# Optimization experiments

Hardware: AMD Instinct MI355X
Metric: run time of the kernel (lower is better)

## Reference

```python
import jax, jax.numpy as jnp
import numpy as np
from jax import lax

S = 16  # encoder stride (patchify-conv stand-in for the CNN backbone, stride-16 feature grid)


def _conv(x, w, b, stride, padding):
    y = lax.conv_general_dilated(x, w, (stride, stride), padding,
                                 dimension_numbers=('NCHW', 'OIHW', 'NCHW'))
    return y + b[None, :, None, None]


def _l2norm(x, eps=1e-12):  # F.normalize(p=2, dim=1)
    n = jnp.sqrt(jnp.sum(x * x, axis=1, keepdims=True))
    return x / jnp.maximum(n, eps)


def _encode(frame, ew, eb, kw, kb, vw, vb, mask=None):
    feat = jax.nn.relu(_conv(frame, ew, eb, S, 'VALID'))  # [B,512,h,w]
    key = _conv(feat, kw, kb, 1, 'SAME')                  # [B,64,h,w]
    val = _conv(feat, vw, vb, 1, 'SAME')                  # [B,ed,h,w]
    if mask is not None:
        m = mask[:, None, ::S, ::S]  # torch F.interpolate 'nearest' with exact integer factor
        key = key * m
        val = val * m
    return _l2norm(key), val, feat


def _forward(query_frame, prev_frame, prev_mask, first_frame, first_mask,
             enc_q_w, enc_q_b, enc_m_w, enc_m_b,
             key_w, key_b, val_w, val_b,
             dec1_w, dec1_b, dec2_w, dec2_b, cls_w, cls_b):
    # memory bank reset + push(first), push(prev)
    k1, v1, _ = _encode(first_frame, enc_m_w, enc_m_b, key_w, key_b, val_w, val_b, first_mask)
    kp, vp, _ = _encode(prev_frame, enc_m_w, enc_m_b, key_w, key_b, val_w, val_b, prev_mask)
    qk, qv, _ = _encode(query_frame, enc_q_w, enc_q_b, key_w, key_b, val_w, val_b)
    B, Ck, h, w = qk.shape
    ed = qv.shape[1]
    mem_key = jnp.concatenate([k1.reshape(B, Ck, -1), kp.reshape(B, Ck, -1)], axis=2)  # [B,64,M]
    mem_val = jnp.concatenate([v1.reshape(B, ed, -1), vp.reshape(B, ed, -1)], axis=2)  # [B,ed,M]
    q_key = qk.reshape(B, Ck, -1)                                                      # [B,64,Q]
    # STM memory read: affinity -> softmax -> weighted sum over memory pixels
    affinity = jnp.einsum('bcq,bcm->bqm', q_key, mem_key) / jnp.sqrt(jnp.float32(Ck))
    affinity = jax.nn.softmax(affinity, axis=-1)
    mem_read = jnp.einsum('bqm,bcm->bcq', affinity, mem_val).reshape(B, ed, h, w)
    fused = jnp.concatenate([qv, mem_read], axis=1)  # [B,2*ed,h,w] (aspp=False)
    d = jax.nn.relu(_conv(fused, dec1_w, dec1_b, 1, 'SAME'))
    dec_feat = jax.nn.relu(_conv(d, dec2_w, dec2_b, 1, 'SAME'))
    logits = _conv(dec_feat, cls_w, cls_b, 1, 'SAME')
    H, W = query_frame.shape[-2], query_frame.shape[-1]
    logits_full = jax.image.resize(logits, (B, logits.shape[1], H, W), method='bilinear')  # align_corners=False
    rep_feat = _l2norm(dec_feat)
    return rep_feat, logits_full


def setup_inputs():
    key = jax.random.key(0)
    ks = jax.random.split(key, 16)
    B, H, W = 8, 512, 512
    Ce, Ck, ed = 512, 64, 256
    g = lambda i, sh, s: jax.random.normal(ks[i], sh, dtype=jnp.float32) * s
    return {
        'query_frame': g(0, (B, 3, H, W), 1.0),
        'prev_frame': g(1, (B, 3, H, W), 1.0),
        'prev_mask': jnp.round(jax.random.uniform(ks[2], (B, H, W), dtype=jnp.float32)),
        'first_frame': g(3, (B, 3, H, W), 1.0),
        'first_mask': jnp.round(jax.random.uniform(ks[4], (B, H, W), dtype=jnp.float32)),
        'enc_q_w': g(5, (Ce, 3, S, S), 0.02), 'enc_q_b': jnp.zeros((Ce,), jnp.float32),
        'enc_m_w': g(6, (Ce, 3, S, S), 0.02), 'enc_m_b': jnp.zeros((Ce,), jnp.float32),
        'key_w': g(7, (Ck, Ce, 1, 1), 0.05), 'key_b': jnp.zeros((Ck,), jnp.float32),
        'val_w': g(8, (ed, Ce, 1, 1), 0.05), 'val_b': jnp.zeros((ed,), jnp.float32),
        'dec1_w': g(9, (ed, 2 * ed, 3, 3), 0.02), 'dec1_b': jnp.zeros((ed,), jnp.float32),
        'dec2_w': g(10, (ed, ed, 3, 3), 0.02), 'dec2_b': jnp.zeros((ed,), jnp.float32),
        'cls_w': g(11, (2, ed, 1, 1), 0.05), 'cls_b': jnp.zeros((2,), jnp.float32),
    }


def reference(query_frame, prev_frame, prev_mask, first_frame, first_mask,
              enc_q_w, enc_q_b, enc_m_w, enc_m_b,
              key_w, key_b, val_w, val_b,
              dec1_w, dec1_b, dec2_w, dec2_b, cls_w, cls_b):
    return _forward(query_frame, prev_frame, prev_mask, first_frame, first_mask,
                    enc_q_w, enc_q_b, enc_m_w, enc_m_b,
                    key_w, key_b, val_w, val_b,
                    dec1_w, dec1_b, dec2_w, dec2_b, cls_w, cls_b)
```

## Files before the change

kernel.cpp:

```cpp
#include <hip/hip_runtime.h>
#include <hip/hip_bf16.h>
#include <cstdint>

#define DEV __device__ __forceinline__
typedef __attribute__((ext_vector_type(8))) short short8;
typedef __attribute__((ext_vector_type(4))) float f32x4;
typedef unsigned short u16;

DEV float b2f(u16 u) { union { unsigned int i; float f; } x; x.i = (unsigned)u << 16; return x.f; }
DEV u16 f2b(float f) { __hip_bfloat16 h = __float2bfloat16(f); return *(u16*)&h; }
DEV float rdin(const void* p, size_t i, int isbf) {
  return isbf ? __bfloat162float(((const __hip_bfloat16*)p)[i]) : ((const float*)p)[i];
}
DEV void wrout(void* p, size_t i, float v, int isbf) {
  if (isbf) ((__hip_bfloat16*)p)[i] = __float2bfloat16(v);
  else      ((float*)p)[i] = v;
}
DEV short8 ld8(const void* p, size_t idx, int isbf) {
  if (isbf) return *(const short8*)((const u16*)p + idx);
  const float* f = (const float*)p + idx;
  float4 x = *(const float4*)f, y = *(const float4*)(f + 4);
  short8 r;
  r[0] = f2b(x.x); r[1] = f2b(x.y); r[2] = f2b(x.z); r[3] = f2b(x.w);
  r[4] = f2b(y.x); r[5] = f2b(y.y); r[6] = f2b(y.z); r[7] = f2b(y.w);
  return r;
}

__global__ __launch_bounds__(256) void detect_k(const u16* w, int* flag) {
  __shared__ int cnt[256];
  int tid = threadIdx.x, c = 0;
  for (int i = tid; i < 4096; i += 256) {
    u16 v = w[i];
    int e = (v >> 7) & 0xFF;
    if (v == 0 || (e >= 0x60 && e <= 0x9F)) c++;
  }
  cnt[tid] = c;
  __syncthreads();
  for (int s = 128; s > 0; s >>= 1) { if (tid < s) cnt[tid] += cnt[tid + s]; __syncthreads(); }
  if (tid == 0) *flag = (cnt[0] > 3600) ? 1 : 0;
}

__global__ __launch_bounds__(256) void patchify_k(const void* F0, const void* F1,
                                                  u16* dst, const int* dflag) {
  int isbf = *dflag;
  int bid = blockIdx.x;
  int z = bid >> 8, rem = bid & 255, b = rem >> 5, y = rem & 31;
  const void* F = z ? F1 : F0;
  int x = threadIdx.x & 31, pj = threadIdx.x >> 5;
  u16* drow = dst + (size_t)(z * 8192 + b * 1024 + y * 32 + x) * 768;
#pragma unroll
  for (int i = 0; i < 6; i++) {
    int pair = i * 8 + pj;
    int c = pair >> 4, ky = pair & 15;
    size_t src = ((size_t)((b * 3 + c) * 512 + y * 16 + ky)) * 512 + x * 16;
    short8 v0 = ld8(F, src, isbf);
    short8 v1 = ld8(F, src + 8, isbf);
    u16* dp = drow + c * 256 + ky * 16;
    *(short8*)dp = v0;
    *(short8*)(dp + 8) = v1;
  }
}

__global__ __launch_bounds__(256) void wconv_k(const void* wm, const void* wq,
                                               u16* dst, const int* dflag) {
  int isbf = *dflag;
  size_t e0 = ((size_t)blockIdx.x * 256 + threadIdx.x) * 8;
  const void* src = e0 < 393216 ? wm : wq;
  size_t off = e0 < 393216 ? e0 : e0 - 393216;
  *(short8*)&dst[e0] = ld8(src, off, isbf);
}

struct PA {
  const void* W0; const void* W1; size_t bs; int K; int rowsplit; int zsel; int ws16; int rowmax1;
  DEV short8 l8(int row, int k, int b, int zz, int isbf) const {
    const void* W = W0; int r = row;
    if (zsel && zz == 2) W = W1;
    else if (rowsplit && row >= rowsplit) { W = W1; r = row - rowsplit; if (r > rowmax1) r = rowmax1; }
    return ld8(W, (size_t)b * bs + (size_t)r * K + k, ws16 ? 1 : isbf);
  }
};
struct PBws {
  const u16* X; int rs; size_t zs;
  DEV short8 l8(int t, int k, int zz, int) const {
    return *(const short8*)(X + (size_t)zz * zs + (size_t)t * rs + k);
  }
};
struct PBc3 {
  const u16* X; int C; int shift;
  DEV short8 l8(int t, int k, int, int) const {
    int tap = k >> shift, c0 = k & (C - 1);
    int dy = tap / 3, dx = tap - dy * 3;
    int pos = t & 1023, y = pos >> 5, x = pos & 31;
    int iy = y + dy - 1, ix = x + dx - 1;
    if ((unsigned)iy >= 32u || (unsigned)ix >= 32u) { short8 z = {0,0,0,0,0,0,0,0}; return z; }
    return *(const short8*)(X + (size_t)(((t >> 10) * 1024) + iy * 32 + ix) * C + c0);
  }
};

struct Epi {
  int mode;
  u16 *o16, *o16b, *o16c;
  size_t zs; int ts, moff, mmax;
  const void *bias, *bias2; int bzsel;
  const void *maskA, *maskB;
  const float* rscale;
  float scale; int relu, doexp;
  DEV void store1(int m, int t, int z, float v, int isbf) const {
    if (m >= mmax) return;
    int b = t >> 10, pos = t & 1023;
    if (m < 256) {
      v += rdin(bias, m, isbf);
      if (z < 2) {
        const void* mk = z ? maskB : maskA;
        v *= rdin(mk, ((size_t)(b * 512 + (pos >> 5) * 16) << 9) + (pos & 31) * 16, isbf);
        o16[((size_t)(b * 256 + m)) * 2048 + (size_t)z * 1024 + pos] = f2b(v);
      } else {
        o16b[(size_t)t * 512 + m] = f2b(v);
      }
    } else {
      v += rdin(bias2, m - 256, isbf);
      o16c[((size_t)z * 8192 + t) * 64 + (m - 256)] = f2b(v);
    }
  }
};

template <class PB>
__global__ __launch_bounds__(256) void mg(PA pa, PB pb, Epi ep, int ktiles, int nbase,
                                          int ksplit, const int* dflag) {
  __shared__ u16 sh[16384];
  u16* As = sh; u16* Bs = sh + 8192;
  int isbf = *dflag;
  int tid = threadIdx.x, lane = tid & 63;
  int col16 = lane & 15, quad = lane >> 4;
  int wv = tid >> 6, wm = wv >> 1, wn = wv & 1;
  int zz = blockIdx.z;
  int kb = ksplit * zz;
  int n0 = blockIdx.x * 128, m0 = blockIdx.y * 128;
  int bA = (nbase + n0) >> 10;

  f32x4 acc[4][4];
#pragma unroll
  for (int mt = 0; mt < 4; mt++)
#pragma unroll
    for (int nt = 0; nt < 4; nt++)
#pragma unroll
      for (int r = 0; r < 4; r++) acc[mt][nt][r] = 0.f;

  int rA[4], lA[4];
#pragma unroll
  for (int g = 0; g < 4; g++) {
    rA[g] = g * 32 + (tid >> 3);
    lA[g] = (tid & 7) ^ (rA[g] & 7);
  }

  short8 ra[4], rb[4];
#pragma unroll
  for (int g = 0; g < 4; g++) {
    ra[g] = pa.l8(m0 + rA[g], kb + lA[g] * 8, bA, zz, isbf);
    rb[g] = pb.l8(nbase + n0 + rA[g], kb + lA[g] * 8, zz, isbf);
  }

  for (int kt = 0; kt < ktiles; kt++) {
    if (kt) __syncthreads();
#pragma unroll
    for (int g = 0; g < 4; g++) {
      *(short8*)&As[(size_t)(g * 256 + tid) * 8] = ra[g];
      *(short8*)&Bs[(size_t)(g * 256 + tid) * 8] = rb[g];
    }
    __syncthreads();
    if (kt + 1 < ktiles) {
      int kn = kb + (kt + 1) * 64;
#pragma unroll
      for (int g = 0; g < 4; g++) {
        ra[g] = pa.l8(m0 + rA[g], kn + lA[g] * 8, bA, zz, isbf);
        rb[g] = pb.l8(nbase + n0 + rA[g], kn + lA[g] * 8, zz, isbf);
      }
    }
#pragma unroll
    for (int s = 0; s < 2; s++) {
      short8 af[4], bf[4];
      int cs = ((s * 4 + quad) ^ (col16 & 7)) << 3;
#pragma unroll
      for (int mt = 0; mt < 4; mt++)
        af[mt] = *(const short8*)&As[(wm * 64 + mt * 16 + col16) * 64 + cs];
#pragma unroll
      for (int nt = 0; nt < 4; nt++)
        bf[nt] = *(const short8*)&Bs[(wn * 64 + nt * 16 + col16) * 64 + cs];
#pragma unroll
      for (int mt = 0; mt < 4; mt++)
#pragma unroll
        for (int nt = 0; nt < 4; nt++)
          acc[mt][nt] = __builtin_amdgcn_mfma_f32_16x16x32_bf16(af[mt], bf[nt], acc[mt][nt], 0, 0, 0);
    }
  }

  if (ep.mode == 1) {
#pragma unroll
    for (int mt = 0; mt < 4; mt++)
#pragma unroll
      for (int nt = 0; nt < 4; nt++)
#pragma unroll
        for (int r = 0; r < 4; r++) {
          int m = m0 + wm * 64 + mt * 16 + quad * 4 + r;
          int t = nbase + n0 + wn * 64 + nt * 16 + col16;
          ep.store1(m, t, zz, acc[mt][nt][r], isbf);
        }
    return;
  }
  if (ep.mode == 2) {
    float* pf = (float*)ep.o16;
#pragma unroll
    for (int mt = 0; mt < 4; mt++)
#pragma unroll
      for (int nt = 0; nt < 4; nt++)
#pragma unroll
        for (int r = 0; r < 4; r++) {
          int m = m0 + wm * 64 + mt * 16 + quad * 4 + r;
          int t = nbase + n0 + wn * 64 + nt * 16 + col16;
          pf[((size_t)(zz * 256 + m)) * 8192 + t] = acc[mt][nt][r];
        }
    return;
  }
  u16* T = sh;
  const int TS = 132;
  for (int p = 0; p < 2; p++) {
    __syncthreads();
    if (wn == p) {
#pragma unroll
      for (int mt = 0; mt < 4; mt++)
#pragma unroll
        for (int nt = 0; nt < 4; nt++) {
          int tl = nt * 16 + col16;
          int tg = nbase + n0 + p * 64 + tl;
#pragma unroll
          for (int r2 = 0; r2 < 2; r2++) {
            int ml = wm * 64 + mt * 16 + quad * 4 + r2 * 2;
            float v0 = acc[mt][nt][r2 * 2] * ep.scale;
            float v1 = acc[mt][nt][r2 * 2 + 1] * ep.scale;
            if (ep.bias) {
              const void* bp = (ep.bzsel && zz == 2) ? ep.bias2 : ep.bias;
              v0 += rdin(bp, m0 + ml, isbf);
              v1 += rdin(bp, m0 + ml + 1, isbf);
            }
            if (ep.doexp) { v0 = __expf(v0); v1 = __expf(v1); }
            if (ep.rscale) { float rs = ep.rscale[tg]; v0 *= rs; v1 *= rs; }
            if (ep.relu) { v0 = fmaxf(v0, 0.f); v1 = fmaxf(v1, 0.f); }
            unsigned int pk = (unsigned)f2b(v0) | ((unsigned)f2b(v1) << 16);
            *(unsigned int*)&T[tl * TS + ml] = pk;
          }
        }
    }
    __syncthreads();
    {
      int tl = tid >> 2, seg = tid & 3;
      int tg = nbase + n0 + p * 64 + tl;
      u16* op = ep.o16 + (size_t)zz * ep.zs + (size_t)tg * ep.ts + ep.moff + m0;
#pragma unroll
      for (int i = 0; i < 4; i++) {
        int c8 = seg + i * 4;
        short8 v = *(short8*)&T[tl * TS + c8 * 8];
        *(short8*)&op[c8 * 8] = v;
      }
    }
  }
}

__global__ __launch_bounds__(256) void comb_k(const float* pf, const void* bias,
                                              u16* out, const int* dflag) {
  int isbf = *dflag;
  int tid = threadIdx.x;
  int t = blockIdx.x * 64 + (tid & 63);
  int mb = (tid >> 6) << 6;
#pragma unroll
  for (int mi = 0; mi < 64; mi += 8) {
    short8 o;
#pragma unroll
    for (int j = 0; j < 8; j++) {
      int m = mb + mi + j;
      float v = pf[(size_t)m * 8192 + t] + pf[(size_t)(m + 256) * 8192 + t];
      v += rdin(bias, m, isbf);
      o[j] = f2b(fmaxf(v, 0.f));
    }
    *(short8*)&out[(size_t)t * 256 + mb + mi] = o;
  }
}

__global__ __launch_bounds__(256) void wreorder_k(const void* src, u16* dst, int C,
                                                  int total, const int* dflag) {
  int idx = blockIdx.x * 256 + threadIdx.x;
  if (idx >= total) return;
  int isbf = *dflag;
  int nine_c = 9 * C;
  int m = idx / nine_c; int r = idx - m * nine_c;
  int tp = r / C; int c = r - tp * C;
  dst[idx] = f2b(rdin(src, (size_t)(m * C + c) * 9 + tp, isbf));
}

__global__ __launch_bounds__(256) void keyfix_k(const u16* kraw3, const void* mA,
                                                const void* mB, u16* memk, u16* qk,
                                                const int* dflag) {
  int isbf = *dflag;
  int z = blockIdx.y;
  int n = blockIdx.x * 256 + threadIdx.x;
  int b = n >> 10, pos = n & 1023;
  float mv = 1.f;
  if (z == 0) mv = rdin(mA, ((size_t)(b * 512 + (pos >> 5) * 16) << 9) + (pos & 31) * 16, isbf);
  else if (z == 1) mv = rdin(mB, ((size_t)(b * 512 + (pos >> 5) * 16) << 9) + (pos & 31) * 16, isbf);
  const u16* src = kraw3 + ((size_t)z * 8192 + n) * 64;
  float v[64], ss = 0.f;
#pragma unroll
  for (int c = 0; c < 64; c++) { v[c] = b2f(src[c]) * mv; ss += v[c] * v[c]; }
  float inv = 1.f / fmaxf(sqrtf(ss), 1e-12f);
  u16* dst = (z < 2) ? memk + (size_t)(b * 2048 + z * 1024 + pos) * 64 : qk + (size_t)n * 64;
#pragma unroll
  for (int c = 0; c < 64; c++) dst[c] = f2b(v[c] * inv);
}

__global__ __launch_bounds__(256) void stats_k(const u16* P, float* rsinv) {
  int tid = threadIdx.x, lane = tid & 63, wv = tid >> 6;
  int row = blockIdx.x * 4 + wv;
  const u16* p = P + (size_t)row * 2048;
  float s = 0.f;
#pragma unroll
  for (int c = 0; c < 4; c++) {
    short8 v = *(const short8*)(p + c * 512 + lane * 8);
#pragma unroll
    for (int j = 0; j < 8; j++) s += b2f((u16)v[j]);
  }
#pragma unroll
  for (int off = 32; off > 0; off >>= 1) s += __shfl_down(s, off);
  if (lane == 0) rsinv[row] = 1.f / s;
}

__global__ __launch_bounds__(256) void repcls_k(const u16* decf, const void* cwgt,
                                                const void* cbias, void* out_rep,
                                                float* logits, const int* dflag) {
  int isbf = *dflag;
  int tid = threadIdx.x, lane = tid & 63, wv = tid >> 6;
  int tok = blockIdx.x * 4 + wv;
  int b = tok >> 10, pos = tok & 1023;
  const u16* src = decf + (size_t)tok * 256;
  int c0 = lane * 4;
  float v[4], ss = 0.f, a0 = 0.f, a1 = 0.f;
#pragma unroll
  for (int j = 0; j < 4; j++) {
    float x = b2f(src[c0 + j]);
    v[j] = x; ss += x * x;
    a0 = fmaf(x, rdin(cwgt, c0 + j, isbf), a0);
    a1 = fmaf(x, rdin(cwgt, 256 + c0 + j, isbf), a1);
  }
#pragma unroll
  for (int off = 32; off > 0; off >>= 1) {
    ss += __shfl_down(ss, off); a0 += __shfl_down(a0, off); a1 += __shfl_down(a1, off);
  }
  ss = __shfl(ss, 0); a0 = __shfl(a0, 0); a1 = __shfl(a1, 0);
  float inv = 1.f / fmaxf(sqrtf(ss), 1e-12f);
#pragma unroll
  for (int j = 0; j < 4; j++)
    wrout(out_rep, ((size_t)(b * 256 + c0 + j) << 10) + pos, v[j] * inv, isbf);
  if (lane == 0) {
    logits[((size_t)(b * 2) << 10) + pos]     = a0 + rdin(cbias, 0, isbf);
    logits[((size_t)(b * 2 + 1) << 10) + pos] = a1 + rdin(cbias, 1, isbf);
  }
}

__global__ __launch_bounds__(256) void resize_k(const float* logits, void* out,
                                                size_t ebase, const int* dflag) {
  int isbf = *dflag;
  int idx = blockIdx.x * 256 + threadIdx.x;
  int ox = idx & 511, oy = (idx >> 9) & 511, c = (idx >> 18) & 1, b = idx >> 19;
  float fy = (oy + 0.5f) * 0.0625f - 0.5f;
  float fx = (ox + 0.5f) * 0.0625f - 0.5f;
  int y0 = (int)floorf(fy), x0 = (int)floorf(fx);
  float wy = fy - y0, wx = fx - x0;
  int y0c = max(y0, 0), y1c = min(y0 + 1, 31);
  int x0c = max(x0, 0), x1c = min(x0 + 1, 31);
  const float* L = logits + ((size_t)(b * 2 + c) << 10);
  float v00 = L[y0c * 32 + x0c], v01 = L[y0c * 32 + x1c];
  float v10 = L[y1c * 32 + x0c], v11 = L[y1c * 32 + x1c];
  float v = (1.f - wy) * ((1.f - wx) * v00 + wx * v01) + wy * ((1.f - wx) * v10 + wx * v11);
  wrout(out, ebase + (size_t)idx, v, isbf);
}

extern "C" void kernel_launch(void* const* d_in, const int* in_sizes, int n_in,
                              void* d_out, int out_size, void* d_ws, size_t ws_size,
                              hipStream_t stream) {
  const void* query  = d_in[0];  const void* prev   = d_in[1];
  const void* prevM  = d_in[2];  const void* first  = d_in[3];
  const void* firstM = d_in[4];  const void* encQw  = d_in[5];
  const void* encQb  = d_in[6];  const void* encMw  = d_in[7];
  const void* encMb  = d_in[8];  const void* keyW   = d_in[9];
  const void* keyB   = d_in[10]; const void* valW   = d_in[11];
  const void* valB   = d_in[12]; const void* dec1W  = d_in[13];
  const void* dec1B  = d_in[14]; const void* dec2W  = d_in[15];
  const void* dec2B  = d_in[16]; const void* clsW   = d_in[17];
  const void* clsB   = d_in[18];

  u16* W = (u16*)d_ws;
  int* dflag = (int*)W;
  float* rsinv  = (float*)(W + 16);
  float* logits = (float*)(W + 16400);
  u16* B0 = W + 49168;
  u16* Xp    = B0;
  u16* feat3 = B0 + 12582912;
  u16* encWb = B0 + 25165824;
  u16* wr1   = B0;
  u16* wr2   = B0 + 1179648;
  u16* fused = B0 + 1769472;
  u16* memv  = B0 + 5963776;
  u16* memk  = B0 + 10158080;
  u16* qk    = B0 + 11206656;
  u16* kraw3 = B0 + 25165824;
  u16* P     = B0 + 11730944;
  float* pf  = (float*)(B0 + 11730944);
  u16* dbuf  = memv;
  u16* decf  = memv + 2097152;

  dim3 blk(256);
  detect_k<<<dim3(1), blk, 0, stream>>>((const u16*)encQw, dflag);

  wconv_k<<<dim3(384), blk, 0, stream>>>(encMw, encQw, encWb, dflag);
  patchify_k<<<dim3(512), blk, 0, stream>>>(first, prev, Xp, dflag);
  {
    PA a{encWb, 0, 0, 768, 0, 0, 1, 0};
    PBws b{Xp, 768, (size_t)8192 * 768};
    Epi e{0, feat3, 0, 0, (size_t)8192 * 512, 512, 0, 512,
          encMb, 0, 0, 0, 0, 0, 1.f, 1, 0};
    mg<PBws><<<dim3(64, 4, 2), blk, 0, stream>>>(a, b, e, 12, 0, 0, dflag);
  }
  patchify_k<<<dim3(256), blk, 0, stream>>>(query, query, Xp, dflag);
  {
    PA a{encWb + 393216, 0, 0, 768, 0, 0, 1, 0};
    PBws b{Xp, 768, 0};
    Epi e{0, feat3 + (size_t)2 * 8192 * 512, 0, 0, 0, 512, 0, 512,
          encQb, 0, 0, 0, 0, 0, 1.f, 1, 0};
    mg<PBws><<<dim3(64, 4, 1), blk, 0, stream>>>(a, b, e, 12, 0, 0, dflag);
  }

  wreorder_k<<<dim3(4608), blk, 0, stream>>>(dec1W, wr1, 512, 256 * 4608, dflag);
  wreorder_k<<<dim3(2304), blk, 0, stream>>>(dec2W, wr2, 256, 256 * 2304, dflag);

  {
    PA a{valW, keyW, 0, 512, 256, 0, 0, 63};
    PBws b{feat3, 512, (size_t)8192 * 512};
    Epi e{1, memv, fused, kraw3, 0, 0, 0, 320,
          valB, keyB, 0, firstM, prevM, 0, 1.f, 0, 0};
    mg<PBws><<<dim3(64, 3, 3), blk, 0, stream>>>(a, b, e, 8, 0, 0, dflag);
  }
  keyfix_k<<<dim3(32, 3), blk, 0, stream>>>(kraw3, firstM, prevM, memk, qk, dflag);

  {
    PA a{memk, 0, 131072, 64, 0, 0, 1, 0};
    PBws b{qk, 64, 0};
    Epi e{0, P, 0, 0, 0, 2048, 0, 1 << 30,
          0, 0, 0, 0, 0, 0, 0.125f, 0, 1};
    mg<PBws><<<dim3(64, 16, 1), blk, 0, stream>>>(a, b, e, 1, 0, 0, dflag);
  }
  stats_k<<<dim3(2048), blk, 0, stream>>>(P, rsinv);
  {
    PA a{memv, 0, 524288, 2048, 0, 0, 1, 0};
    PBws b{P, 2048, 0};
    Epi e{0, fused, 0, 0, 0, 512, 256, 1 << 30,
          0, 0, 0, 0, 0, rsinv, 1.f, 0, 0};
    mg<PBws><<<dim3(64, 2, 1), blk, 0, stream>>>(a, b, e, 32, 0, 0, dflag);
  }

  {
    PA a{wr1, 0, 0, 4608, 0, 0, 1, 0};
    PBc3 b{fused, 512, 9};
    Epi e{2, (u16*)pf, 0, 0, 0, 0, 0, 0,
          0, 0, 0, 0, 0, 0, 1.f, 0, 0};
    mg<PBc3><<<dim3(64, 2, 2), blk, 0, stream>>>(a, b, e, 36, 0, 2304, dflag);
    comb_k<<<dim3(128), blk, 0, stream>>>(pf, dec1B, dbuf, dflag);
  }
  {
    PA a{wr2, 0, 0, 2304, 0, 0, 1, 0};
    PBc3 b{dbuf, 256, 8};
    Epi e{2, (u16*)pf, 0, 0, 0, 0, 0, 0,
          0, 0, 0, 0, 0, 0, 1.f, 0, 0};
    mg<PBc3><<<dim3(64, 2, 2), blk, 0, stream>>>(a, b, e, 18, 0, 1152, dflag);
    comb_k<<<dim3(128), blk, 0, stream>>>(pf, dec2B, decf, dflag);
  }

  repcls_k<<<dim3(2048), blk, 0, stream>>>(decf, clsW, clsB, d_out, logits, dflag);
  resize_k<<<dim3(16384), blk, 0, stream>>>(logits, d_out, (size_t)2097152, dflag);
}
```

Before: 505.2 us.

## Double-buffer GEMM LDS tiles, fuse softmax row sums, split dec1 K four ways

The shared GEMM kernel gets a templated double-buffered LDS scheme, which removes one barrier per k-tile by alternating between two tile buffers. The softmax row-sum stats kernel is dropped: the affinity GEMM epilogue accumulates exp sums with atomics into a buffer zeroed in wconv_k, and the readout GEMM inverts them. The dec1 conv uses a 4-way K split instead of 2-way for more parallelism, and comb_k is generalised to sum N partials. The trade-offs are doubled LDS per block, which lowers occupancy, plus atomic contention and extra partial-sum traffic.

```diff
diff --git a/kernel.cpp b/kernel.cpp
--- a/kernel.cpp
+++ b/kernel.cpp
@@ -62,9 +62,11 @@
 }
 
 __global__ __launch_bounds__(256) void wconv_k(const void* wm, const void* wq,
-                                               u16* dst, const int* dflag) {
-  int isbf = *dflag;
-  size_t e0 = ((size_t)blockIdx.x * 256 + threadIdx.x) * 8;
+                                               u16* dst, float* rsum, const int* dflag) {
+  int isbf = *dflag;
+  int gi = blockIdx.x * 256 + threadIdx.x;
+  if (gi < 8192) rsum[gi] = 0.f;
+  size_t e0 = (size_t)gi * 8;
   const void* src = e0 < 393216 ? wm : wq;
   size_t off = e0 < 393216 ? e0 : e0 - 393216;
   *(short8*)&dst[e0] = ld8(src, off, isbf);
@@ -105,6 +107,8 @@
   const void *maskA, *maskB;
   const float* rscale;
   float scale; int relu, doexp;
+  float* rsum;
+  int rinv;
   DEV void store1(int m, int t, int z, float v, int isbf) const {
     if (m >= mmax) return;
     int b = t >> 10, pos = t & 1023;
@@ -124,11 +128,10 @@
   }
 };
 
-template <class PB>
+template <class PB, int NBUF>
 __global__ __launch_bounds__(256) void mg(PA pa, PB pb, Epi ep, int ktiles, int nbase,
                                           int ksplit, const int* dflag) {
-  __shared__ u16 sh[16384];
-  u16* As = sh; u16* Bs = sh + 8192;
+  __shared__ u16 sh[NBUF * 16384];
   int isbf = *dflag;
   int tid = threadIdx.x, lane = tid & 63;
   int col16 = lane & 15, quad = lane >> 4;
@@ -159,16 +162,18 @@
     ra[g] = pa.l8(m0 + rA[g], kb + lA[g] * 8, bA, zz, isbf);
     rb[g] = pb.l8(nbase + n0 + rA[g], kb + lA[g] * 8, zz, isbf);
   }
+#pragma unroll
+  for (int g = 0; g < 4; g++) {
+    *(short8*)&sh[(size_t)(g * 256 + tid) * 8] = ra[g];
+    *(short8*)&sh[8192 + (size_t)(g * 256 + tid) * 8] = rb[g];
+  }
+  __syncthreads();
 
   for (int kt = 0; kt < ktiles; kt++) {
-    if (kt) __syncthreads();
-#pragma unroll
-    for (int g = 0; g < 4; g++) {
-      *(short8*)&As[(size_t)(g * 256 + tid) * 8] = ra[g];
-      *(short8*)&Bs[(size_t)(g * 256 + tid) * 8] = rb[g];
-    }
-    __syncthreads();
-    if (kt + 1 < ktiles) {
+    const u16* As = sh + ((NBUF == 2 && (kt & 1)) ? 16384 : 0);
+    const u16* Bs = As + 8192;
+    bool more = (kt + 1 < ktiles);
+    if (more) {
       int kn = kb + (kt + 1) * 64;
 #pragma unroll
       for (int g = 0; g < 4; g++) {
@@ -191,6 +196,16 @@
 #pragma unroll
         for (int nt = 0; nt < 4; nt++)
           acc[mt][nt] = __builtin_amdgcn_mfma_f32_16x16x32_bf16(af[mt], bf[nt], acc[mt][nt], 0, 0, 0);
+    }
+    if (more) {
+      u16* An = sh + ((NBUF == 2 && !(kt & 1)) ? 16384 : 0);
+      if (NBUF == 1) __syncthreads();
+#pragma unroll
+      for (int g = 0; g < 4; g++) {
+        *(short8*)&An[(size_t)(g * 256 + tid) * 8] = ra[g];
+        *(short8*)&An[8192 + (size_t)(g * 256 + tid) * 8] = rb[g];
+      }
+      __syncthreads();
     }
   }
 
@@ -221,11 +236,12 @@
         }
     return;
   }
-  u16* T = sh;
+  u16* T = (u16*)sh;
   const int TS = 132;
   for (int p = 0; p < 2; p++) {
     __syncthreads();
     if (wn == p) {
+      float tsum[4] = {0.f, 0.f, 0.f, 0.f};
 #pragma unroll
       for (int mt = 0; mt < 4; mt++)
 #pragma unroll
@@ -243,12 +259,22 @@
               v1 += rdin(bp, m0 + ml + 1, isbf);
             }
             if (ep.doexp) { v0 = __expf(v0); v1 = __expf(v1); }
-            if (ep.rscale) { float rs = ep.rscale[tg]; v0 *= rs; v1 *= rs; }
+            if (ep.rscale) {
+              float rs = ep.rscale[tg];
+              if (ep.rinv) rs = 1.f / rs;
+              v0 *= rs; v1 *= rs;
+            }
             if (ep.relu) { v0 = fmaxf(v0, 0.f); v1 = fmaxf(v1, 0.f); }
+            if (ep.rsum) tsum[nt] += v0 + v1;
             unsigned int pk = (unsigned)f2b(v0) | ((unsigned)f2b(v1) << 16);
             *(unsigned int*)&T[tl * TS + ml] = pk;
           }
         }
+      if (ep.rsum) {
+#pragma unroll
+        for (int nt = 0; nt < 4; nt++)
+          atomicAdd(&ep.rsum[nbase + n0 + p * 64 + nt * 16 + col16], tsum[nt]);
+      }
     }
     __syncthreads();
     {
@@ -266,22 +292,28 @@
 }
 
 __global__ __launch_bounds__(256) void comb_k(const float* pf, const void* bias,
-                                              u16* out, const int* dflag) {
+                                              u16* out, int ts, int moff, int npart,
+                                              int relu, const float* rsum,
+                                              const int* dflag) {
   int isbf = *dflag;
   int tid = threadIdx.x;
   int t = blockIdx.x * 64 + (tid & 63);
   int mb = (tid >> 6) << 6;
+  float rs = rsum ? 1.f / rsum[t] : 1.f;
 #pragma unroll
   for (int mi = 0; mi < 64; mi += 8) {
     short8 o;
 #pragma unroll
     for (int j = 0; j < 8; j++) {
       int m = mb + mi + j;
-      float v = pf[(size_t)m * 8192 + t] + pf[(size_t)(m + 256) * 8192 + t];
-      v += rdin(bias, m, isbf);
-      o[j] = f2b(fmaxf(v, 0.f));
-    }
-    *(short8*)&out[(size_t)t * 256 + mb + mi] = o;
+      float v = pf[(size_t)m * 8192 + t];
+      for (int p = 1; p < npart; p++) v += pf[(size_t)(p * 256 + m) * 8192 + t];
+      v *= rs;
+      if (bias) v += rdin(bias, m, isbf);
+      if (relu) v = fmaxf(v, 0.f);
+      o[j] = f2b(v);
+    }
+    *(short8*)&out[(size_t)t * ts + moff + mb + mi] = o;
   }
 }
 
@@ -314,22 +346,6 @@
   u16* dst = (z < 2) ? memk + (size_t)(b * 2048 + z * 1024 + pos) * 64 : qk + (size_t)n * 64;
 #pragma unroll
   for (int c = 0; c < 64; c++) dst[c] = f2b(v[c] * inv);
-}
-
-__global__ __launch_bounds__(256) void stats_k(const u16* P, float* rsinv) {
-  int tid = threadIdx.x, lane = tid & 63, wv = tid >> 6;
-  int row = blockIdx.x * 4 + wv;
-  const u16* p = P + (size_t)row * 2048;
-  float s = 0.f;
-#pragma unroll
-  for (int c = 0; c < 4; c++) {
-    short8 v = *(const short8*)(p + c * 512 + lane * 8);
-#pragma unroll
-    for (int j = 0; j < 8; j++) s += b2f((u16)v[j]);
-  }
-#pragma unroll
-  for (int off = 32; off > 0; off >>= 1) s += __shfl_down(s, off);
-  if (lane == 0) rsinv[row] = 1.f / s;
 }
 
 __global__ __launch_bounds__(256) void repcls_k(const u16* decf, const void* cwgt,
@@ -398,7 +414,7 @@
 
   u16* W = (u16*)d_ws;
   int* dflag = (int*)W;
-  float* rsinv  = (float*)(W + 16);
+  float* rsum   = (float*)(W + 16);
   float* logits = (float*)(W + 16400);
   u16* B0 = W + 49168;
   u16* Xp    = B0;
@@ -419,14 +435,14 @@
   dim3 blk(256);
   detect_k<<<dim3(1), blk, 0, stream>>>((const u16*)encQw, dflag);
 
-  wconv_k<<<dim3(384), blk, 0, stream>>>(encMw, encQw, encWb, dflag);
+  wconv_k<<<dim3(384), blk, 0, stream>>>(encMw, encQw, encWb, rsum, dflag);
   patchify_k<<<dim3(512), blk, 0, stream>>>(first, prev, Xp, dflag);
   {
     PA a{encWb, 0, 0, 768, 0, 0, 1, 0};
     PBws b{Xp, 768, (size_t)8192 * 768};
     Epi e{0, feat3, 0, 0, (size_t)8192 * 512, 512, 0, 512,
           encMb, 0, 0, 0, 0, 0, 1.f, 1, 0};
-    mg<PBws><<<dim3(64, 4, 2), blk, 0, stream>>>(a, b, e, 12, 0, 0, dflag);
+    mg<PBws, 2><<<dim3(64, 4, 2), blk, 0, stream>>>(a, b, e, 12, 0, 0, dflag);
   }
   patchify_k<<<dim3(256), blk, 0, stream>>>(query, query, Xp, dflag);
   {
@@ -434,7 +450,7 @@
     PBws b{Xp, 768, 0};
     Epi e{0, feat3 + (size_t)2 * 8192 * 512, 0, 0, 0, 512, 0, 512,
           encQb, 0, 0, 0, 0, 0, 1.f, 1, 0};
-    mg<PBws><<<dim3(64, 4, 1), blk, 0, stream>>>(a, b, e, 12, 0, 0, dflag);
+    mg<PBws, 2><<<dim3(64, 4, 1), blk, 0, stream>>>(a, b, e, 12, 0, 0, dflag);
   }
 
   wreorder_k<<<dim3(4608), blk, 0, stream>>>(dec1W, wr1, 512, 256 * 4608, dflag);
@@ -445,7 +461,7 @@
     PBws b{feat3, 512, (size_t)8192 * 512};
     Epi e{1, memv, fused, kraw3, 0, 0, 0, 320,
           valB, keyB, 0, firstM, prevM, 0, 1.f, 0, 0};
-    mg<PBws><<<dim3(64, 3, 3), blk, 0, stream>>>(a, b, e, 8, 0, 0, dflag);
+    mg<PBws, 2><<<dim3(64, 3, 3), blk, 0, stream>>>(a, b, e, 8, 0, 0, dflag);
   }
   keyfix_k<<<dim3(32, 3), blk, 0, stream>>>(kraw3, firstM, prevM, memk, qk, dflag);
 
@@ -453,16 +469,15 @@
     PA a{memk, 0, 131072, 64, 0, 0, 1, 0};
     PBws b{qk, 64, 0};
     Epi e{0, P, 0, 0, 0, 2048, 0, 1 << 30,
-          0, 0, 0, 0, 0, 0, 0.125f, 0, 1};
-    mg<PBws><<<dim3(64, 16, 1), blk, 0, stream>>>(a, b, e, 1, 0, 0, dflag);
-  }
-  stats_k<<<dim3(2048), blk, 0, stream>>>(P, rsinv);
+          0, 0, 0, 0, 0, 0, 0.125f, 0, 1, rsum, 0};
+    mg<PBws, 1><<<dim3(64, 16, 1), blk, 0, stream>>>(a, b, e, 1, 0, 0, dflag);
+  }
   {
     PA a{memv, 0, 524288, 2048, 0, 0, 1, 0};
     PBws b{P, 2048, 0};
     Epi e{0, fused, 0, 0, 0, 512, 256, 1 << 30,
-          0, 0, 0, 0, 0, rsinv, 1.f, 0, 0};
-    mg<PBws><<<dim3(64, 2, 1), blk, 0, stream>>>(a, b, e, 32, 0, 0, dflag);
+          0, 0, 0, 0, 0, rsum, 1.f, 0, 0, 0, 1};
+    mg<PBws, 2><<<dim3(64, 2, 1), blk, 0, stream>>>(a, b, e, 32, 0, 0, dflag);
   }
 
   {
@@ -470,16 +485,16 @@
     PBc3 b{fused, 512, 9};
     Epi e{2, (u16*)pf, 0, 0, 0, 0, 0, 0,
           0, 0, 0, 0, 0, 0, 1.f, 0, 0};
-    mg<PBc3><<<dim3(64, 2, 2), blk, 0, stream>>>(a, b, e, 36, 0, 2304, dflag);
-    comb_k<<<dim3(128), blk, 0, stream>>>(pf, dec1B, dbuf, dflag);
+    mg<PBc3, 2><<<dim3(64, 2, 4), blk, 0, stream>>>(a, b, e, 18, 0, 1152, dflag);
+    comb_k<<<dim3(128), blk, 0, stream>>>(pf, dec1B, dbuf, 256, 0, 4, 1, 0, dflag);
   }
   {
     PA a{wr2, 0, 0, 2304, 0, 0, 1, 0};
     PBc3 b{dbuf, 256, 8};
     Epi e{2, (u16*)pf, 0, 0, 0, 0, 0, 0,
           0, 0, 0, 0, 0, 0, 1.f, 0, 0};
-    mg<PBc3><<<dim3(64, 2, 2), blk, 0, stream>>>(a, b, e, 18, 0, 1152, dflag);
-    comb_k<<<dim3(128), blk, 0, stream>>>(pf, dec2B, decf, dflag);
+    mg<PBc3, 2><<<dim3(64, 2, 2), blk, 0, stream>>>(a, b, e, 18, 0, 1152, dflag);
+    comb_k<<<dim3(128), blk, 0, stream>>>(pf, dec2B, decf, 256, 0, 2, 1, 0, dflag);
   }
 
   repcls_k<<<dim3(2048), blk, 0, stream>>>(decf, clsW, clsB, d_out, logits, dflag);
```

Measured after the change: 606.0 us. 19.9% more time.
